# Optimization experiments

Measured on AMD Instinct MI355X. Metric: run time of the kernel, lower is better.

Reference implementation:

```python
import math
import jax, jax.numpy as jnp
import numpy as np

B = 32768
DM = 256      # d_model
DS = 16       # d_state
DI = 256      # d_inner (expand=1)
DTR = 16      # dt_rank = ceil(256/16)
FF = 512      # FFN hidden


def setup_inputs() -> dict:
    key = jax.random.key(0)
    ks = jax.random.split(key, 10)
    def rn(k, sh, s=0.02):
        return jax.random.normal(k, sh, jnp.float32) * s
    return {
        "x_0": jax.random.uniform(ks[0], (B, 4), jnp.float32),
        "flow_features": jax.random.normal(ks[1], (B, 1, DM), jnp.float32),
        "h": jnp.zeros((B, DI, DS), jnp.float32),
        "W_in": rn(ks[2], (2 * DI, DM)),
        "W_x": rn(ks[3], (DTR + 2 * DS, DI)),
        "W_dt": rn(ks[4], (DI, DTR)),
        "b_dt": jnp.zeros((DI,), jnp.float32),
        "A_log": jnp.log(jnp.broadcast_to(jnp.arange(1, DS + 1, dtype=jnp.float32), (DI, DS))),
        "D": jnp.ones((DI,), jnp.float32),
        "W1": rn(ks[5], (FF, DM)),
        "b1": jnp.zeros((FF,), jnp.float32),
        "W2": rn(ks[6], (DM, FF)),
        "b2": jnp.zeros((DM,), jnp.float32),
        "gamma": jnp.ones((DM,), jnp.float32),
        "beta": jnp.zeros((DM,), jnp.float32),
        "W_bb": rn(ks[7], (4, DM)),
        "b_bb": jnp.zeros((4,), jnp.float32),
    }


def _sine_embed(pos, dim_per_axis):
    # Matches gen_sineembed_for_position for pos.shape[-1]==4 (cx, cy, w, h order)
    dim_t = 10000.0 ** (2.0 * (jnp.arange(dim_per_axis) // 2).astype(jnp.float32) / dim_per_axis)
    scale = 2.0 * math.pi
    def emb(v):  # v: (b,)
        p = v[:, None] * scale / dim_t          # (b, dim)
        return jnp.stack([jnp.sin(p[:, 0::2]), jnp.cos(p[:, 1::2])], axis=2).reshape(v.shape[0], dim_per_axis)
    return jnp.concatenate([emb(pos[:, 0]), emb(pos[:, 1]), emb(pos[:, 2]), emb(pos[:, 3])], axis=1)


def reference(x_0, flow_features, h, W_in, W_x, W_dt, b_dt, A_log, D,
              W1, b1, W2, b2, gamma, beta, W_bb, b_bb):
    # 1) sinusoidal bbox embedding -> (b, d_model)
    pos = _sine_embed(x_0, DM // 4)
    # 2) in_proj + split + SiLU (l==1 so sequence dim is collapsed)
    pm = pos @ W_in.T                              # (b, 2*d_inner)
    u, gate = pm[:, :DI], pm[:, DI:]
    u = jax.nn.silu(u)
    # 3) input-dependent SSM params from flow_features (l==1)
    x_dbl = flow_features[:, 0] @ W_x.T            # (b, dt_rank + 2n)
    dlt = x_dbl[:, :DTR]
    Bm = x_dbl[:, DTR:DTR + DS]                    # (b, n)
    Cm = x_dbl[:, DTR + DS:]                       # (b, n)
    delta = jax.nn.softplus(dlt @ W_dt.T + b_dt)   # (b, d_in)
    A = -jnp.exp(A_log)                            # (d_in, n)
    # 4) single selective-scan step
    deltaA = jnp.exp(delta[:, :, None] * A)                      # (b, d_in, n)
    deltaBu = delta[:, :, None] * Bm[:, None, :] * u[:, :, None] # (b, d_in, n)
    h_new = deltaA * h + deltaBu                                 # (b, d_in, n)
    y = jnp.einsum('bdn,bn->bd', h_new, Cm) + u * D              # (b, d_in)
    # 5) gated SiLU
    y = y * jax.nn.silu(gate)                                    # (b, d_model)
    # 6) FFN + residual + LayerNorm
    src2 = jax.nn.relu(y @ W1.T + b1) @ W2.T + b2
    s = y + src2
    mu = s.mean(-1, keepdims=True)
    var = s.var(-1, keepdims=True)
    s = (s - mu) / jnp.sqrt(var + 1e-5) * gamma + beta
    # 7) bbox head + sigmoid
    out = jax.nn.sigmoid(s @ W_bb.T + b_bb)                      # (b, 4)
    return (out, h_new)
```

## Files before the change

### kernel.cpp

```cpp
#include <hip/hip_runtime.h>
#include <math.h>

#define B_TOT 32768
#define DM    256
#define DS    16
#define DI    256
#define DTR   16
#define FF    512
#define ROWS  32
#define STA   260

__device__ __forceinline__ float sigmoidf_(float x) { return 1.0f / (1.0f + __expf(-x)); }

extern "C" __global__ void __launch_bounds__(256, 4)
mamba_fused(const float* __restrict__ x0,
            const float* __restrict__ flow,
            const float* __restrict__ hin,
            const float* __restrict__ W_in,
            const float* __restrict__ W_x,
            const float* __restrict__ W_dt,
            const float* __restrict__ b_dt,
            const float* __restrict__ A_log,
            const float* __restrict__ Dp,
            const float* __restrict__ W1,
            const float* __restrict__ b1,
            const float* __restrict__ W2,
            const float* __restrict__ b2,
            const float* __restrict__ gamma,
            const float* __restrict__ beta,
            const float* __restrict__ W_bb,
            const float* __restrict__ b_bb,
            float* __restrict__ out,
            float* __restrict__ h_new)
{
    __shared__ __align__(16) float sA[ROWS * STA];
    __shared__ __align__(16) float sU[ROWS * 48];
    __shared__ float sX0[ROWS * 4];
    __shared__ float sMu[ROWS], sRstd[ROWS];

    const int t = threadIdx.x;
    const size_t g0 = (size_t)blockIdx.x * ROWS;

    if (t < ROWS * 4) sX0[t] = x0[g0 * 4 + t];
    __syncthreads();

    {
        const int c = t & 63, axis = t >> 6;
        const float f = 6.28318530717958647692f * __expf(-(float)(c >> 1) * 0.2878231366242557f);
        #pragma unroll
        for (int r = 0; r < ROWS; ++r) {
            float p = sX0[r * 4 + axis] * f;
            sA[r * STA + t] = (c & 1) ? __cosf(p) : __sinf(p);
        }
    }

    for (int idx = t; idx < ROWS * 48; idx += 256) {
        const int r = idx / 48, j = idx - r * 48;
        const float4* fv = (const float4*)(flow + (g0 + r) * DM);
        const float4* wv = (const float4*)(W_x + (size_t)j * DM);
        float acc = 0.f;
        #pragma unroll 8
        for (int k = 0; k < DM / 4; ++k) {
            float4 a = fv[k], b = wv[k];
            acc += a.x * b.x + a.y * b.y + a.z * b.z + a.w * b.w;
        }
        sU[idx] = acc;
    }
    __syncthreads();

    float2 ug[ROWS];
    {
        float acc0[ROWS], acc1[ROWS];
        #pragma unroll
        for (int r = 0; r < ROWS; ++r) { acc0[r] = 0.f; acc1[r] = 0.f; }
        const float4* w0v = (const float4*)(W_in + (size_t)t * DM);
        const float4* w1v = (const float4*)(W_in + (size_t)(t + DI) * DM);
        #pragma unroll 2
        for (int kc = 0; kc < DM / 4; ++kc) {
            float4 w0 = w0v[kc], w1 = w1v[kc];
            #pragma unroll
            for (int r = 0; r < ROWS; ++r) {
                float4 p = *(const float4*)&sA[r * STA + kc * 4];
                acc0[r] += p.x * w0.x + p.y * w0.y + p.z * w0.z + p.w * w0.w;
                acc1[r] += p.x * w1.x + p.y * w1.y + p.z * w1.z + p.w * w1.w;
            }
        }
        #pragma unroll
        for (int r = 0; r < ROWS; ++r) {
            float a = acc0[r], g = acc1[r];
            ug[r].x = a * sigmoidf_(a);
            ug[r].y = g * sigmoidf_(g);
        }
    }

    float Wdt_row[DTR], Arow[DS];
    #pragma unroll
    for (int k = 0; k < DTR; ++k) Wdt_row[k] = W_dt[t * DTR + k];
    #pragma unroll
    for (int n = 0; n < DS; ++n) Arow[n] = -__expf(A_log[t * DS + n]);
    const float bdt = b_dt[t];
    const float Dt = Dp[t];

    __syncthreads();

    #pragma unroll
    for (int r = 0; r < ROWS; ++r) {
        const size_t hbase = ((g0 + r) * DI + t) * DS;
        const float4* hv = (const float4*)(hin + hbase);
        float hi[16];
        *(float4*)&hi[0]  = hv[0];
        *(float4*)&hi[4]  = hv[1];
        *(float4*)&hi[8]  = hv[2];
        *(float4*)&hi[12] = hv[3];
        const float* xd = &sU[r * 48];
        float d = bdt;
        #pragma unroll
        for (int k = 0; k < DTR; ++k) d += xd[k] * Wdt_row[k];
        d = (d > 20.f) ? d : __logf(1.f + __expf(d));
        const float uvv = ug[r].x;
        const float du = d * uvv;
        float ysum = 0.f;
        #pragma unroll
        for (int n = 0; n < DS; ++n) {
            float dA = __expf(d * Arow[n]);
            float v = dA * hi[n] + du * xd[16 + n];
            hi[n] = v;
            ysum += v * xd[32 + n];
        }
        float4* ho = (float4*)(h_new + hbase);
        ho[0] = *(const float4*)&hi[0];
        ho[1] = *(const float4*)&hi[4];
        ho[2] = *(const float4*)&hi[8];
        ho[3] = *(const float4*)&hi[12];
        sA[r * STA + t] = (ysum + uvv * Dt) * ug[r].y;
    }
    __syncthreads();

    float acc2[ROWS];
    #pragma unroll
    for (int r = 0; r < ROWS; ++r) acc2[r] = 0.f;
    const int rr = t >> 3;
    const int j4 = (t & 7) * 4;
    for (int jc = 0; jc < FF; jc += 32) {
        float fa[4];
        #pragma unroll
        for (int q = 0; q < 4; ++q) fa[q] = b1[jc + j4 + q];
        #pragma unroll 2
        for (int kc = 0; kc < DM / 4; ++kc) {
            float4 yv4 = *(const float4*)&sA[rr * STA + kc * 4];
            #pragma unroll
            for (int q = 0; q < 4; ++q) {
                float4 w = *(const float4*)&W1[(size_t)(jc + j4 + q) * DM + kc * 4];
                fa[q] += yv4.x * w.x + yv4.y * w.y + yv4.z * w.z + yv4.w * w.w;
            }
        }
        float4 f4;
        f4.x = fmaxf(fa[0], 0.f); f4.y = fmaxf(fa[1], 0.f);
        f4.z = fmaxf(fa[2], 0.f); f4.w = fmaxf(fa[3], 0.f);
        *(float4*)&sU[rr * 32 + j4] = f4;
        __syncthreads();
        const float4* w2v = (const float4*)(W2 + (size_t)t * FF + jc);
        #pragma unroll
        for (int jj = 0; jj < 8; ++jj) {
            float4 w = w2v[jj];
            #pragma unroll
            for (int r = 0; r < ROWS; ++r) {
                float4 fv4 = *(const float4*)&sU[r * 32 + jj * 4];
                acc2[r] += fv4.x * w.x + fv4.y * w.y + fv4.z * w.z + fv4.w * w.w;
            }
        }
        __syncthreads();
    }

    {
        const float b2t = b2[t];
        #pragma unroll
        for (int r = 0; r < ROWS; ++r) sA[r * STA + t] += acc2[r] + b2t;
    }
    __syncthreads();

    {
        const int r = t >> 3, q = t & 7;
        float s1 = 0.f, s2s = 0.f;
        #pragma unroll
        for (int k4 = 0; k4 < 8; ++k4) {
            float4 v = *(const float4*)&sA[r * STA + q * 32 + k4 * 4];
            s1  += v.x + v.y + v.z + v.w;
            s2s += v.x * v.x + v.y * v.y + v.z * v.z + v.w * v.w;
        }
        s1 += __shfl_xor(s1, 1);  s2s += __shfl_xor(s2s, 1);
        s1 += __shfl_xor(s1, 2);  s2s += __shfl_xor(s2s, 2);
        s1 += __shfl_xor(s1, 4);  s2s += __shfl_xor(s2s, 4);
        if (q == 0) {
            const float mu  = s1 * (1.f / DM);
            const float var = s2s * (1.f / DM) - mu * mu;
            sMu[r]   = mu;
            sRstd[r] = rsqrtf(var + 1e-5f);
        }
    }
    __syncthreads();

    {
        const int r = t >> 3, c = (t >> 1) & 3, hf = t & 1;
        const float mu = sMu[r], rstd = sRstd[r];
        float acc = 0.f;
        const int i0 = hf * 128;
        #pragma unroll 8
        for (int i4 = 0; i4 < 32; ++i4) {
            const int i = i0 + i4 * 4;
            float4 sv = *(const float4*)&sA[r * STA + i];
            float4 gm = *(const float4*)&gamma[i];
            float4 bt = *(const float4*)&beta[i];
            float4 wb = *(const float4*)&W_bb[c * DM + i];
            acc += ((sv.x - mu) * rstd * gm.x + bt.x) * wb.x
                 + ((sv.y - mu) * rstd * gm.y + bt.y) * wb.y
                 + ((sv.z - mu) * rstd * gm.z + bt.z) * wb.z
                 + ((sv.w - mu) * rstd * gm.w + bt.w) * wb.w;
        }
        acc += __shfl_xor(acc, 1);
        if (hf == 0) out[(g0 + r) * 4 + c] = sigmoidf_(acc + b_bb[c]);
    }
}

extern "C" void kernel_launch(void* const* d_in, const int* in_sizes, int n_in,
                              void* d_out, int out_size, void* d_ws, size_t ws_size,
                              hipStream_t stream) {
    const float* x0    = (const float*)d_in[0];
    const float* flow  = (const float*)d_in[1];
    const float* hin   = (const float*)d_in[2];
    const float* W_in  = (const float*)d_in[3];
    const float* W_x   = (const float*)d_in[4];
    const float* W_dt  = (const float*)d_in[5];
    const float* b_dt  = (const float*)d_in[6];
    const float* A_log = (const float*)d_in[7];
    const float* Dp    = (const float*)d_in[8];
    const float* W1    = (const float*)d_in[9];
    const float* b1    = (const float*)d_in[10];
    const float* W2    = (const float*)d_in[11];
    const float* b2    = (const float*)d_in[12];
    const float* gamma = (const float*)d_in[13];
    const float* beta  = (const float*)d_in[14];
    const float* W_bb  = (const float*)d_in[15];
    const float* b_bb  = (const float*)d_in[16];

    float* out   = (float*)d_out;
    float* h_new = out + (size_t)B_TOT * 4;

    dim3 grid(B_TOT / ROWS), block(256);
    hipLaunchKernelGGL(mamba_fused, grid, block, 0, stream,
                       x0, flow, hin, W_in, W_x, W_dt, b_dt, A_log, Dp,
                       W1, b1, W2, b2, gamma, beta, W_bb, b_bb, out, h_new);
}
```

Before: 3.126 ms.

## Split in_proj and scan into two row halves with prefetched h loads

The in_proj GEMM and selective-scan step now run in two chunks of 16 rows instead of 32. This halves the live accumulator registers so the kernel can hold the occupancy requested through amdgpu_waves_per_eu. The scan loop double-buffers the h state, issuing the next row's global load before computing the current row to hide memory latency. In exchange, W_in rows are streamed from memory twice and an extra barrier is added per chunk.

```diff
diff --git a/kernel.cpp b/kernel.cpp
--- a/kernel.cpp
+++ b/kernel.cpp
@@ -8,11 +8,12 @@
 #define DTR   16
 #define FF    512
 #define ROWS  32
+#define RH    16
 #define STA   260
 
 __device__ __forceinline__ float sigmoidf_(float x) { return 1.0f / (1.0f + __expf(-x)); }
 
-extern "C" __global__ void __launch_bounds__(256, 4)
+extern "C" __attribute__((amdgpu_waves_per_eu(4, 4))) __global__ void __launch_bounds__(256)
 mamba_fused(const float* __restrict__ x0,
             const float* __restrict__ flow,
             const float* __restrict__ hin,
@@ -68,71 +69,88 @@
     }
     __syncthreads();
 
-    float2 ug[ROWS];
-    {
-        float acc0[ROWS], acc1[ROWS];
-        #pragma unroll
-        for (int r = 0; r < ROWS; ++r) { acc0[r] = 0.f; acc1[r] = 0.f; }
-        const float4* w0v = (const float4*)(W_in + (size_t)t * DM);
-        const float4* w1v = (const float4*)(W_in + (size_t)(t + DI) * DM);
-        #pragma unroll 2
-        for (int kc = 0; kc < DM / 4; ++kc) {
-            float4 w0 = w0v[kc], w1 = w1v[kc];
-            #pragma unroll
-            for (int r = 0; r < ROWS; ++r) {
-                float4 p = *(const float4*)&sA[r * STA + kc * 4];
-                acc0[r] += p.x * w0.x + p.y * w0.y + p.z * w0.z + p.w * w0.w;
-                acc1[r] += p.x * w1.x + p.y * w1.y + p.z * w1.z + p.w * w1.w;
-            }
-        }
-        #pragma unroll
-        for (int r = 0; r < ROWS; ++r) {
-            float a = acc0[r], g = acc1[r];
-            ug[r].x = a * sigmoidf_(a);
-            ug[r].y = g * sigmoidf_(g);
-        }
-    }
-
-    float Wdt_row[DTR], Arow[DS];
-    #pragma unroll
-    for (int k = 0; k < DTR; ++k) Wdt_row[k] = W_dt[t * DTR + k];
-    #pragma unroll
-    for (int n = 0; n < DS; ++n) Arow[n] = -__expf(A_log[t * DS + n]);
     const float bdt = b_dt[t];
     const float Dt = Dp[t];
 
-    __syncthreads();
-
-    #pragma unroll
-    for (int r = 0; r < ROWS; ++r) {
-        const size_t hbase = ((g0 + r) * DI + t) * DS;
-        const float4* hv = (const float4*)(hin + hbase);
-        float hi[16];
-        *(float4*)&hi[0]  = hv[0];
-        *(float4*)&hi[4]  = hv[1];
-        *(float4*)&hi[8]  = hv[2];
-        *(float4*)&hi[12] = hv[3];
-        const float* xd = &sU[r * 48];
-        float d = bdt;
-        #pragma unroll
-        for (int k = 0; k < DTR; ++k) d += xd[k] * Wdt_row[k];
-        d = (d > 20.f) ? d : __logf(1.f + __expf(d));
-        const float uvv = ug[r].x;
-        const float du = d * uvv;
-        float ysum = 0.f;
-        #pragma unroll
-        for (int n = 0; n < DS; ++n) {
-            float dA = __expf(d * Arow[n]);
-            float v = dA * hi[n] + du * xd[16 + n];
-            hi[n] = v;
-            ysum += v * xd[32 + n];
-        }
-        float4* ho = (float4*)(h_new + hbase);
-        ho[0] = *(const float4*)&hi[0];
-        ho[1] = *(const float4*)&hi[4];
-        ho[2] = *(const float4*)&hi[8];
-        ho[3] = *(const float4*)&hi[12];
-        sA[r * STA + t] = (ysum + uvv * Dt) * ug[r].y;
+    for (int cch = 0; cch < 2; ++cch) {
+        const int rb = cch * RH;
+
+        float u[RH], gs[RH];
+        {
+            float acc0[RH], acc1[RH];
+            #pragma unroll
+            for (int r = 0; r < RH; ++r) { acc0[r] = 0.f; acc1[r] = 0.f; }
+            const float4* w0v = (const float4*)(W_in + (size_t)t * DM);
+            const float4* w1v = (const float4*)(W_in + (size_t)(t + DI) * DM);
+            #pragma unroll 2
+            for (int kc = 0; kc < DM / 4; ++kc) {
+                float4 w0 = w0v[kc], w1 = w1v[kc];
+                #pragma unroll
+                for (int r = 0; r < RH; ++r) {
+                    float4 p = *(const float4*)&sA[(rb + r) * STA + kc * 4];
+                    acc0[r] += p.x * w0.x + p.y * w0.y + p.z * w0.z + p.w * w0.w;
+                    acc1[r] += p.x * w1.x + p.y * w1.y + p.z * w1.z + p.w * w1.w;
+                }
+            }
+            #pragma unroll
+            for (int r = 0; r < RH; ++r) {
+                float a = acc0[r], g = acc1[r];
+                u[r]  = a * sigmoidf_(a);
+                gs[r] = g * sigmoidf_(g);
+            }
+        }
+
+        float Wdt_row[DTR], Arow[DS];
+        #pragma unroll
+        for (int k = 0; k < DTR; ++k) Wdt_row[k] = W_dt[t * DTR + k];
+        #pragma unroll
+        for (int n = 0; n < DS; ++n) Arow[n] = -__expf(A_log[t * DS + n]);
+
+        __syncthreads();
+
+        float hp[2][16];
+        {
+            const size_t hb0 = ((g0 + rb) * DI + t) * DS;
+            const float4* hv = (const float4*)(hin + hb0);
+            *(float4*)&hp[0][0]  = hv[0];
+            *(float4*)&hp[0][4]  = hv[1];
+            *(float4*)&hp[0][8]  = hv[2];
+            *(float4*)&hp[0][12] = hv[3];
+        }
+        #pragma unroll
+        for (int r = 0; r < RH; ++r) {
+            const int cur = r & 1, nxt = cur ^ 1;
+            if (r + 1 < RH) {
+                const size_t hb = ((g0 + rb + r + 1) * DI + t) * DS;
+                const float4* hv = (const float4*)(hin + hb);
+                *(float4*)&hp[nxt][0]  = hv[0];
+                *(float4*)&hp[nxt][4]  = hv[1];
+                *(float4*)&hp[nxt][8]  = hv[2];
+                *(float4*)&hp[nxt][12] = hv[3];
+            }
+            const float* xd = &sU[(rb + r) * 48];
+            float d = bdt;
+            #pragma unroll
+            for (int k = 0; k < DTR; ++k) d += xd[k] * Wdt_row[k];
+            d = (d > 20.f) ? d : __logf(1.f + __expf(d));
+            const float uvv = u[r];
+            const float du = d * uvv;
+            float ysum = 0.f;
+            #pragma unroll
+            for (int n = 0; n < DS; ++n) {
+                float dA = __expf(d * Arow[n]);
+                float v = dA * hp[cur][n] + du * xd[16 + n];
+                hp[cur][n] = v;
+                ysum += v * xd[32 + n];
+            }
+            const size_t hb = ((g0 + rb + r) * DI + t) * DS;
+            float4* ho = (float4*)(h_new + hb);
+            ho[0] = *(const float4*)&hp[cur][0];
+            ho[1] = *(const float4*)&hp[cur][4];
+            ho[2] = *(const float4*)&hp[cur][8];
+            ho[3] = *(const float4*)&hp[cur][12];
+            sA[(rb + r) * STA + t] = (ysum + uvv * Dt) * gs[r];
+        }
     }
     __syncthreads();
 
```

Measured after the change: 3.256 ms. 1.04x slower.
